# Optimization experiments

Measured on AMD Instinct MI355X. Metric: run time of the kernel, lower is better.

Reference implementation:

```python
import jax, jax.numpy as jnp
import numpy as np

N, D, V = 4096, 256, 32000
B, T = 32, 256
U_DECAY, X_DECAY = 0.97, 0.97
EPS = 1e-6


def layernorm_row(z):
    # matches torch: (z - mean) / (std + eps), std with Bessel correction (ddof=1)
    m = jnp.mean(z, axis=-1, keepdims=True)
    s = jnp.std(z, axis=-1, keepdims=True, ddof=1)
    return (z - m) / (s + EPS)


def setup_inputs() -> dict:
    key = jax.random.key(0)
    k1, k2, k3, k4, k5 = jax.random.split(key, 5)
    token_emb = jax.random.normal(k1, (V, D), jnp.float32) / np.float32(np.sqrt(D))
    E = jax.random.normal(k2, (D, N), jnp.float32) / np.float32(np.sqrt(N))
    Dx = jax.random.normal(k3, (N, D), jnp.float32) / np.float32(np.sqrt(D))
    Dy = jax.random.normal(k4, (N, D), jnp.float32) / np.float32(np.sqrt(D))
    idx = jax.random.randint(k5, (B, T), 0, V)
    return {"idx": idx, "token_emb": token_emb, "E": E, "Dx": Dx, "Dy": Dy}


def reference(idx, token_emb, E, Dx, Dy):
    b = idx.shape[0]

    def step(carry, tok):
        x, rho = carry                                   # x: (b,n), rho: (b,d,n)
        v_prev = token_emb[tok]                          # (b,d) embedding gather
        x_t = X_DECAY * x + jax.nn.relu(v_prev @ Dx.T)   # (b,n)
        x_t = x_t / (jnp.sum(jnp.abs(x_t), axis=-1, keepdims=True) + EPS)  # L1 normalize
        a_star = jnp.einsum('bdn,bn->bd', rho, x_t)      # fast-weight readout
        y_t = jax.nn.relu(layernorm_row(a_star) @ Dy.T) * jax.nn.relu(x_t)  # (b,n)
        v_star = layernorm_row(y_t @ E.T)                # (b,d)
        # Hebbian decayed outer-product memory update
        rho = U_DECAY * (rho + jnp.einsum('bd,bn->bdn', layernorm_row(v_prev), x_t))
        return (x_t, rho), v_star

    x0 = jnp.zeros((b, N), jnp.float32)
    rho0 = jnp.zeros((b, D, N), jnp.float32)
    (_, _), vs = jax.lax.scan(step, (x0, rho0), idx.T)   # vs: (T,b,d)
    return jnp.transpose(vs, (1, 0, 2))                  # (b,T,d)
```

## Files before the change

kernel.cpp:

```cpp
#include <hip/hip_runtime.h>
#include <hip/hip_bf16.h>

#define NN 4096
#define DD 256
#define BB 32
#define TT 256
#define EPS 1e-6f
#define DECAY 0.97f
#define LOG2_DECAY -0.043943348f

typedef __hip_bfloat16 bf16;
typedef short short8 __attribute__((ext_vector_type(8)));
typedef float floatx4 __attribute__((ext_vector_type(4)));

__device__ __forceinline__ float bfu2f(short u) {
    return __uint_as_float(((unsigned)(unsigned short)u) << 16);
}

__device__ __forceinline__ float blk_sum_256(float v, volatile float* s4) {
#pragma unroll
    for (int o = 32; o > 0; o >>= 1) v += __shfl_down(v, o, 64);
    int lane = threadIdx.x & 63, w = threadIdx.x >> 6;
    __syncthreads();
    if (lane == 0) s4[w] = v;
    __syncthreads();
    return s4[0] + s4[1] + s4[2] + s4[3];
}

__device__ __forceinline__ void gl16(const bf16* g, bf16* l) {
    __builtin_amdgcn_global_load_lds((const __attribute__((address_space(1))) void*)g,
                                     (__attribute__((address_space(3))) void*)l, 16, 0, 0);
}

__global__ void k_detect(const unsigned short* __restrict__ raw, int* __restrict__ flag) {
    __shared__ int cnt[4];
    int tid = threadIdx.x;
    int bad = 0;
    for (int i = tid; i < 8192; i += 256) {
        unsigned int u = raw[2 * i];
        float v = __uint_as_float(u << 16);
        if (!(fabsf(v) < 1e6f)) bad++;
    }
#pragma unroll
    for (int o = 32; o > 0; o >>= 1) bad += __shfl_down(bad, o, 64);
    int lane = tid & 63, w = tid >> 6;
    if (lane == 0) cnt[w] = bad;
    __syncthreads();
    if (tid == 0) flag[0] = (cnt[0] + cnt[1] + cnt[2] + cnt[3] < 32) ? 1 : 0;
}

__global__ __launch_bounds__(256) void k_convert3(const void* __restrict__ s0,
                                                  const void* __restrict__ s1,
                                                  const void* __restrict__ s2,
                                                  bf16* __restrict__ d0,
                                                  bf16* __restrict__ d1,
                                                  bf16* __restrict__ d2,
                                                  const int* __restrict__ flag) {
    const int per = NN * DD / 8;
    int i = blockIdx.x * 256 + threadIdx.x;
    int m = i / per, j = i % per;
    const void* s = (m == 0) ? s0 : (m == 1) ? s1 : s2;
    bf16* d = (m == 0) ? d0 : (m == 1) ? d1 : d2;
    if (flag[0]) {
        ((uint4*)d)[j] = ((const uint4*)s)[j];
    } else {
        const float4* f = (const float4*)s;
        float4 a = f[2 * j], b = f[2 * j + 1];
        short8 o;
        float va[8] = {a.x, a.y, a.z, a.w, b.x, b.y, b.z, b.w};
#pragma unroll
        for (int k = 0; k < 8; k++) {
            bf16 t = __float2bfloat16(va[k]);
            o[k] = *reinterpret_cast<short*>(&t);
        }
        ((short8*)d)[j] = o;
    }
}

__global__ __launch_bounds__(256) void k_gather_ln(const void* __restrict__ emb,
                                                   const int* __restrict__ idx,
                                                   bf16* __restrict__ Vpb,
                                                   bf16* __restrict__ Ub,
                                                   const int* __restrict__ flag) {
    __shared__ float s4[4];
    int r = blockIdx.x, d = threadIdx.x;
    int tok = idx[r];
    long o = (long)tok * DD + d;
    float e = flag[0] ? __bfloat162float(((const bf16*)emb)[o]) : ((const float*)emb)[o];
    Vpb[(long)r * DD + d] = __float2bfloat16(e);
    float m = blk_sum_256(e, s4) * (1.0f / DD);
    float zc = e - m;
    float var = blk_sum_256(zc * zc, s4) * (1.0f / (DD - 1));
    Ub[(long)r * DD + d] = __float2bfloat16(zc / (sqrtf(fmaxf(var, 0.f)) + EPS));
}

__global__ __launch_bounds__(256) void k_transpose(const bf16* __restrict__ Ub,
                                                   bf16* __restrict__ Ut) {
    __shared__ bf16 tile[32][33];
    int b = blockIdx.z;
    int t0 = blockIdx.x * 32, d0 = blockIdx.y * 32;
    const bf16* src = Ub + (long)b * TT * DD;
    bf16* dst = Ut + (long)b * DD * TT;
    int rr = threadIdx.x >> 3, c4 = (threadIdx.x & 7) * 4;
#pragma unroll
    for (int i = 0; i < 4; i++) tile[rr][c4 + i] = src[(long)(t0 + rr) * DD + d0 + c4 + i];
    __syncthreads();
#pragma unroll
    for (int i = 0; i < 4; i++) dst[(long)(d0 + rr) * TT + t0 + c4 + i] = tile[c4 + i][rr];
}

enum { EPI_RELU_BF16 = 0, EPI_NONE_F32 = 1, EPI_RELU_MULX_BF16 = 2, EPI_NONE_BF16 = 3 };

template <int EPI>
__global__ __launch_bounds__(512, 2) void k_fused256(const bf16* __restrict__ A,
                                                     const bf16* __restrict__ B,
                                                     bf16* __restrict__ C,
                                                     const bf16* __restrict__ Xaux,
                                                     float* __restrict__ Wsum) {
    __shared__ __align__(16) char smem[65536];
    bf16* R = (bf16*)smem;

    int bx = blockIdx.x, by = blockIdx.y;
    {
        int gx = gridDim.x;
        int nwg = gx * gridDim.y;
        int id = by * gx + bx;
        int q = nwg >> 3;
        int nid = (id & 7) * q + (id >> 3);
        bx = nid % gx;
        by = nid / gx;
    }
    int bm = by * 256, bn = bx * 256;
    int tid = threadIdx.x, wid = tid >> 6, lane = tid & 63;
    int wr = wid >> 2, wc = wid & 3;
    int lm = lane & 15, kh = lane >> 4;

    int srow2 = tid >> 2;
    int swzcol = (((tid & 3) ^ ((srow2 >> 1) & 3)) << 3);
    const bf16* gA0 = A + (long)(bm + srow2) * DD + swzcol;
    const bf16* gA1 = gA0 + (long)128 * DD;
    const bf16* gB0 = B + (long)(bn + srow2) * DD + swzcol;
    const bf16* gB1 = gB0 + (long)128 * DD;
    int chunk = ((kh ^ ((lm >> 1) & 3)) << 3);

    floatx4 acc[8][4];
#pragma unroll
    for (int i = 0; i < 8; i++)
#pragma unroll
        for (int j = 0; j < 4; j++) acc[i][j] = (floatx4){0.f, 0.f, 0.f, 0.f};

#define STAGE256(SBASE, KK)                             \
    {                                                   \
        bf16* As_ = (bf16*)(SBASE);                     \
        bf16* Bs_ = As_ + 8192;                         \
        gl16(gA0 + (KK), As_ + tid * 8);                \
        gl16(gA1 + (KK), As_ + 4096 + tid * 8);         \
        gl16(gB0 + (KK), Bs_ + tid * 8);                \
        gl16(gB1 + (KK), Bs_ + 4096 + tid * 8);         \
    }

    STAGE256(smem, 0);

    int cur = 0;
#pragma unroll
    for (int k0 = 0; k0 < 256; k0 += 32) {
        __builtin_amdgcn_s_barrier();
        __builtin_amdgcn_sched_barrier(0);
        if (k0 + 32 < 256) STAGE256(smem + ((cur ^ 1) * 32768), k0 + 32);
        if (k0 + 32 < 256) asm volatile("s_waitcnt vmcnt(4)" ::: "memory");
        else               asm volatile("s_waitcnt vmcnt(0)" ::: "memory");
        __builtin_amdgcn_s_barrier();
        __builtin_amdgcn_sched_barrier(0);
        bf16* cbA = (bf16*)(smem + cur * 32768);
        bf16* cbB = cbA + 8192;
        short8 af[8], bfr[4];
#pragma unroll
        for (int i = 0; i < 8; i++)
            af[i] = *(const short8*)(cbA + (wr * 128 + i * 16 + lm) * 32 + chunk);
#pragma unroll
        for (int j = 0; j < 4; j++)
            bfr[j] = *(const short8*)(cbB + (wc * 64 + j * 16 + lm) * 32 + chunk);
#pragma unroll
        for (int i = 0; i < 8; i++)
#pragma unroll
            for (int j = 0; j < 4; j++)
                acc[i][j] = __builtin_amdgcn_mfma_f32_16x16x32_bf16(af[i], bfr[j], acc[i][j], 0, 0, 0);
        cur ^= 1;
    }
#undef STAGE256

#pragma unroll
    for (int p = 0; p < 4; p++) {
        __syncthreads();
        if (wr == (p >> 1)) {
            int ibase = (p & 1) * 4;
#pragma unroll
            for (int ii = 0; ii < 4; ii++)
#pragma unroll
                for (int j = 0; j < 4; j++)
#pragma unroll
                    for (int r = 0; r < 4; r++) {
                        int rr = ii * 16 + kh * 4 + r;
                        int cc = wc * 64 + j * 16 + lm;
                        R[rr * 264 + cc] = __float2bfloat16(fmaxf(acc[ibase + ii][j][r], 0.f));
                    }
        }
        __syncthreads();
#pragma unroll
        for (int it = 0; it < 4; it++) {
            int row_l = it * 16 + (tid >> 5);
            int c8 = (tid & 31) * 8;
            short8 vv = *(const short8*)(R + row_l * 264 + c8);
            int gm = bm + p * 64 + row_l;
            long off = (long)gm * NN + bn + c8;
            if (EPI == EPI_RELU_BF16) {
                *(short8*)(C + off) = vv;
                float s = 0.f;
#pragma unroll
                for (int k = 0; k < 8; k++) s += bfu2f(vv[k]);
#pragma unroll
                for (int o = 16; o > 0; o >>= 1) s += __shfl_down(s, o, 32);
                if ((tid & 31) == 0) atomicAdd(&Wsum[gm], s);
            } else {
                short8 xx = *(const short8*)(Xaux + off);
                short8 oo;
#pragma unroll
                for (int k = 0; k < 8; k++) {
                    float prod = bfu2f(vv[k]) * fmaxf(bfu2f(xx[k]), 0.f);
                    bf16 t = __float2bfloat16(prod);
                    oo[k] = *reinterpret_cast<short*>(&t);
                }
                *(short8*)(C + off) = oo;
            }
        }
    }
}

template <int EPI, int KSPLIT, int TRI, int SWZ>
__global__ __launch_bounds__(256) void k_mfma_nt(int K,
                                                 const bf16* __restrict__ A, int lda, long sA,
                                                 const bf16* __restrict__ B, int ldb, long sB,
                                                 void* __restrict__ Cv, int ldc, long sC,
                                                 const bf16* __restrict__ Xaux,
                                                 float* __restrict__ Wsum) {
    __shared__ __align__(16) char smem[49152];
    bf16* R = (bf16*)smem;

    int z = blockIdx.z;
    int bz = z / KSPLIT, ks = z % KSPLIT;
    A += (long)bz * sA;
    B += (long)bz * sB;
    int bx = blockIdx.x, by = blockIdx.y;
    if (TRI) {
        by = (blockIdx.x >= 1) ? 1 : 0;
        bx = (blockIdx.x == 2) ? 1 : 0;
    }
    if (SWZ) {
        int gx = gridDim.x;
        int nwg = gx * gridDim.y;
        int id = by * gx + bx;
        int q = nwg >> 3;
        int nid = (id & 7) * q + (id >> 3);
        bx = nid % gx;
        by = nid / gx;
    }
    int bm = by * 128, bn = bx * 128;
    int tid = threadIdx.x;
    int srow = tid >> 2;
    int scol = ((((srow >> 1) & 3) ^ (tid & 3)) << 3);
    int w = tid >> 6, lane = tid & 63;
    int wm = (w >> 1) * 64, wn = (w & 1) * 64;
    int lm = lane & 15, kh = lane >> 4;

    floatx4 acc[4][4];
#pragma unroll
    for (int i = 0; i < 4; i++)
#pragma unroll
        for (int j = 0; j < 4; j++) acc[i][j] = (floatx4){0.f, 0.f, 0.f, 0.f};

    int kchunk = K / KSPLIT;
    int kbeg = ks * kchunk, kend = kbeg + kchunk;
    const bf16* gA0 = A + (long)(bm + srow) * lda + scol;
    const bf16* gA1 = gA0 + (long)64 * lda;
    const bf16* gB0 = B + (long)(bn + srow) * ldb + scol;
    const bf16* gB1 = gB0 + (long)64 * ldb;
    int dslot = tid * 8;

#define STAGE_SLOT(SBASE, KK)                          \
    {                                                  \
        bf16* bufA = (bf16*)(SBASE);                   \
        bf16* bufB = bufA + 4096;                      \
        gl16(gA0 + (KK), bufA + dslot);                \
        gl16(gA1 + (KK), bufA + 2048 + dslot);         \
        gl16(gB0 + (KK), bufB + dslot);                \
        gl16(gB1 + (KK), bufB + 2048 + dslot);         \
    }

    STAGE_SLOT(smem, kbeg);
    if (kbeg + 32 < kend) STAGE_SLOT(smem + 16384, kbeg + 32);

    int cur = 0;
    for (int k0 = kbeg; k0 < kend; k0 += 32) {
        __builtin_amdgcn_s_barrier();
        __builtin_amdgcn_sched_barrier(0);
        if (k0 + 64 < kend) {
            int ps = (cur == 0) ? 2 : cur - 1;
            STAGE_SLOT(smem + ps * 16384, k0 + 64);
        }
        int rem = (kend - k0 - 32) >> 5;
        if (rem >= 2)      asm volatile("s_waitcnt vmcnt(8)" ::: "memory");
        else if (rem == 1) asm volatile("s_waitcnt vmcnt(4)" ::: "memory");
        else               asm volatile("s_waitcnt vmcnt(0)" ::: "memory");
        __builtin_amdgcn_s_barrier();
        __builtin_amdgcn_sched_barrier(0);
        bf16* cbA = (bf16*)(smem + cur * 16384);
        bf16* cbB = cbA + 4096;
        short8 af[4], bfr[4];
#pragma unroll
        for (int i = 0; i < 4; i++) {
            int row = wm + i * 16 + lm;
            af[i] = *(const short8*)(cbA + row * 32 + ((((row >> 1) & 3) ^ kh) << 3));
        }
#pragma unroll
        for (int j = 0; j < 4; j++) {
            int row = wn + j * 16 + lm;
            bfr[j] = *(const short8*)(cbB + row * 32 + ((((row >> 1) & 3) ^ kh) << 3));
        }
#pragma unroll
        for (int i = 0; i < 4; i++)
#pragma unroll
            for (int j = 0; j < 4; j++)
                acc[i][j] = __builtin_amdgcn_mfma_f32_16x16x32_bf16(af[i], bfr[j], acc[i][j], 0, 0, 0);
        cur = (cur == 2) ? 0 : cur + 1;
    }
#undef STAGE_SLOT

    if (EPI == EPI_NONE_F32) {
        long cbase = (long)z * sC;
#pragma unroll
        for (int i = 0; i < 4; i++)
#pragma unroll
            for (int j = 0; j < 4; j++)
#pragma unroll
                for (int r = 0; r < 4; r++) {
                    int gm = bm + wm + i * 16 + kh * 4 + r;
                    int gn = bn + wn + j * 16 + lm;
                    ((float*)Cv)[cbase + (long)gm * ldc + gn] = acc[i][j][r];
                }
        return;
    }

    bf16* Cb = (bf16*)Cv + (long)z * sC;
#pragma unroll
    for (int p = 0; p < 2; p++) {
        __syncthreads();
        if ((w >> 1) == p) {
#pragma unroll
            for (int i = 0; i < 4; i++)
#pragma unroll
                for (int j = 0; j < 4; j++)
#pragma unroll
                    for (int r = 0; r < 4; r++) {
                        int rr = i * 16 + kh * 4 + r;
                        int cc = wn + j * 16 + lm;
                        float val = acc[i][j][r];
                        if (EPI != EPI_NONE_BF16) val = fmaxf(val, 0.f);
                        R[rr * 136 + cc] = __float2bfloat16(val);
                    }
        }
        __syncthreads();
#pragma unroll
        for (int it = 0; it < 4; it++) {
            int row_l = it * 16 + (tid >> 4);
            int c8 = (tid & 15) * 8;
            short8 vv = *(const short8*)(R + row_l * 136 + c8);
            int gm = bm + p * 64 + row_l;
            long off = (long)gm * ldc + bn + c8;
            if (EPI == EPI_NONE_BF16) {
                *(short8*)(Cb + off) = vv;
            } else if (EPI == EPI_RELU_BF16) {
                *(short8*)(Cb + off) = vv;
                float s = 0.f;
#pragma unroll
                for (int k = 0; k < 8; k++) s += bfu2f(vv[k]);
#pragma unroll
                for (int o = 8; o > 0; o >>= 1) s += __shfl_down(s, o, 16);
                if ((tid & 15) == 0) atomicAdd(&Wsum[gm], s);
            } else {
                short8 xx = *(const short8*)(Xaux + off);
                short8 oo;
#pragma unroll
                for (int k = 0; k < 8; k++) {
                    float prod = bfu2f(vv[k]) * fmaxf(bfu2f(xx[k]), 0.f);
                    bf16 t = __float2bfloat16(prod);
                    oo[k] = *reinterpret_cast<short*>(&t);
                }
                *(short8*)(Cb + off) = oo;
            }
        }
    }
}

__global__ __launch_bounds__(256) void k_scalar_scan(const float* __restrict__ Wsum,
                                                     float* __restrict__ invS) {
    __shared__ float sw[BB * TT];
    for (int i = threadIdx.x; i < BB * TT; i += 256) sw[i] = Wsum[i];
    __syncthreads();
    int b = threadIdx.x;
    if (b < BB) {
        float sig = 0.f;
        for (int t = 0; t < TT; t++) {
            float S = DECAY * sig + sw[b * TT + t];
            float inv = 1.f / (S + EPS);
            invS[b * TT + t] = inv;
            sig = S * inv;
        }
    }
}

__global__ __launch_bounds__(256) void k_colscan(bf16* __restrict__ W,
                                                 const float* __restrict__ invS) {
    __shared__ float sv[TT];
    int b = blockIdx.y;
    sv[threadIdx.x] = invS[b * TT + threadIdx.x];
    __syncthreads();
    int n = blockIdx.x * 256 + threadIdx.x;
    bf16* p = W + (long)b * TT * NN + n;
    float x = 0.f;
    for (int t = 0; t < TT; t++) {
        float w = __bfloat162float(p[(long)t * NN]);
        x = (DECAY * x + w) * sv[t];
        p[(long)t * NN] = __float2bfloat16(x);
    }
}

__global__ __launch_bounds__(256) void k_reduce_mask(const bf16* __restrict__ Gp,
                                                     bf16* __restrict__ G) {
    int r = blockIdx.x;
    int b = r >> 8, t = r & 255;
    int s = threadIdx.x;
    long base = ((long)b * 4) * 65536 + (long)t * 256 + s;
    float v = __bfloat162float(Gp[base]) + __bfloat162float(Gp[base + 65536]) +
              __bfloat162float(Gp[base + 2 * 65536]) + __bfloat162float(Gp[base + 3 * 65536]);
    float o = (s < t) ? v * exp2f((float)(t - s) * LOG2_DECAY) : 0.f;
    G[(long)r * 256 + s] = __float2bfloat16(o);
}

__global__ __launch_bounds__(256) void k_ln_rows(const bf16* __restrict__ Zp,
                                                 bf16* __restrict__ O) {
    __shared__ float s4[4];
    long r = blockIdx.x;
    int d = threadIdx.x;
    long b = r >> 8, t = r & 255;
    long base = (b * 2) * 65536 + t * 256 + d;
    float z = __bfloat162float(Zp[base]) + __bfloat162float(Zp[base + 65536]);
    float m = blk_sum_256(z, s4) * (1.0f / DD);
    float zc = z - m;
    float var = blk_sum_256(zc * zc, s4) * (1.0f / (DD - 1));
    O[r * DD + d] = __float2bfloat16(zc / (sqrtf(fmaxf(var, 0.f)) + EPS));
}

__global__ __launch_bounds__(256) void k_final_ln(const float* __restrict__ Zp,
                                                  void* __restrict__ out,
                                                  const int* __restrict__ flag) {
    __shared__ float s4[4];
    long r = blockIdx.x;
    int d = threadIdx.x;
    const long SL = (long)8192 * 256;
    long o = r * DD + d;
    float z = Zp[o] + Zp[o + SL];
    float m = blk_sum_256(z, s4) * (1.0f / DD);
    float zc = z - m;
    float var = blk_sum_256(zc * zc, s4) * (1.0f / (DD - 1));
    float v = zc / (sqrtf(fmaxf(var, 0.f)) + EPS);
    if (flag[0]) ((bf16*)out)[o] = __float2bfloat16(v);
    else ((float*)out)[o] = v;
}

extern "C" void kernel_launch(void* const* d_in, const int* in_sizes, int n_in,
                              void* d_out, int out_size, void* d_ws, size_t ws_size,
                              hipStream_t stream) {
    const int* idx = (const int*)d_in[0];
    const void* emb = d_in[1];
    const void* E = d_in[2];
    const void* Dx = d_in[3];
    const void* Dy = d_in[4];

    char* base = (char*)d_ws;
    size_t off = 0;
    int* flag = (int*)base; off += 1024;
    bf16* Dxb = (bf16*)(base + off); off += (size_t)NN * DD * 2;
    bf16* Dyb = (bf16*)(base + off); off += (size_t)NN * DD * 2;
    bf16* Eb  = (bf16*)(base + off); off += (size_t)DD * NN * 2;
    bf16* Vpb = (bf16*)(base + off); off += (size_t)BB * TT * DD * 2;
    bf16* Ub  = (bf16*)(base + off); off += (size_t)BB * TT * DD * 2;
    bf16* Ut  = (bf16*)(base + off); off += (size_t)BB * TT * DD * 2;
    float* Wsum = (float*)(base + off); off += (size_t)BB * TT * 4;
    float* invS = (float*)(base + off); off += (size_t)BB * TT * 4;
    bf16* ALNb = (bf16*)(base + off); off += (size_t)BB * TT * DD * 2;
    bf16* G = (bf16*)(base + off); off += (size_t)BB * TT * TT * 2;
    bf16* Gp = (bf16*)(base + off); off += (size_t)4 * BB * TT * TT * 2;
    bf16* Astar = Gp;
    float* Zp = (float*)Gp;
    bf16* Xb = (bf16*)(base + off); off += (size_t)BB * TT * NN * 2;

    const int M = BB * TT;

    k_detect<<<1, 256, 0, stream>>>((const unsigned short*)emb, flag);
    k_convert3<<<3 * NN * DD / 8 / 256, 256, 0, stream>>>(Dx, Dy, E, Dxb, Dyb, Eb, flag);
    k_gather_ln<<<M, 256, 0, stream>>>(emb, idx, Vpb, Ub, flag);
    k_transpose<<<dim3(8, 8, BB), 256, 0, stream>>>(Ub, Ut);

    hipMemsetAsync(Wsum, 0, (size_t)M * 4, stream);

    k_fused256<EPI_RELU_BF16><<<dim3(16, 32), 512, 0, stream>>>(Vpb, Dxb, Xb, nullptr, Wsum);

    k_scalar_scan<<<1, 256, 0, stream>>>(Wsum, invS);
    k_colscan<<<dim3(16, BB, 1), 256, 0, stream>>>(Xb, invS);

    k_mfma_nt<EPI_NONE_BF16, 4, 1, 0><<<dim3(3, 1, BB * 4), 256, 0, stream>>>(
        NN, Xb, NN, (long)TT * NN, Xb, NN, (long)TT * NN, Gp, TT, (long)TT * TT, nullptr, nullptr);
    k_reduce_mask<<<M, 256, 0, stream>>>(Gp, G);

    k_mfma_nt<EPI_NONE_BF16, 2, 0, 0><<<dim3(2, 2, BB * 2), 256, 0, stream>>>(
        TT, G, TT, (long)TT * TT, Ut, TT, (long)DD * TT, Astar, DD, (long)TT * DD, nullptr, nullptr);
    k_ln_rows<<<M, 256, 0, stream>>>(Astar, ALNb);

    k_fused256<EPI_RELU_MULX_BF16><<<dim3(16, 32), 512, 0, stream>>>(ALNb, Dyb, Xb, Xb, nullptr);

    k_mfma_nt<EPI_NONE_F32, 2, 0, 1><<<dim3(2, 64, 2), 256, 0, stream>>>(
        NN, Xb, NN, 0, Eb, NN, 0, Zp, DD, (long)M * DD, nullptr, nullptr);

    k_final_ln<<<M, 256, 0, stream>>>(Zp, d_out, flag);
}
```

Measured before the change: 316.0 us.

## Fuse causal decay mask into Gram epilogue and split-K sum into A* GEMM

Applies the causal decay mask inside the Gram-matrix GEMM epilogue, per split-K partial. The A* GEMM now sums the four partials while loading its A operand, which removes the separate reduce_mask kernel and its G buffer. The new A* kernel uses a triangular-aware grid that skips the upper-right zero block. The ln_rows kernel adds the second K-half only for rows at or past 128. This trades a kernel launch and a full read/write pass for extra global loads inside the GEMM, and each partial is rounded to bf16 before summing.

Result: no change. 321.3 us (median of 2 runs) (+1.7%).

```diff
diff --git a/kernel.cpp b/kernel.cpp
--- a/kernel.cpp
+++ b/kernel.cpp
@@ -15,6 +15,11 @@
 
 __device__ __forceinline__ float bfu2f(short u) {
     return __uint_as_float(((unsigned)(unsigned short)u) << 16);
+}
+
+__device__ __forceinline__ short f2bfu(float f) {
+    bf16 t = __float2bfloat16(f);
+    return *reinterpret_cast<short*>(&t);
 }
 
 __device__ __forceinline__ float blk_sum_256(float v, volatile float* s4) {
@@ -69,10 +74,7 @@
         short8 o;
         float va[8] = {a.x, a.y, a.z, a.w, b.x, b.y, b.z, b.w};
 #pragma unroll
-        for (int k = 0; k < 8; k++) {
-            bf16 t = __float2bfloat16(va[k]);
-            o[k] = *reinterpret_cast<short*>(&t);
-        }
+        for (int k = 0; k < 8; k++) o[k] = f2bfu(va[k]);
         ((short8*)d)[j] = o;
     }
 }
@@ -109,7 +111,8 @@
     for (int i = 0; i < 4; i++) dst[(long)(d0 + rr) * TT + t0 + c4 + i] = tile[c4 + i][rr];
 }
 
-enum { EPI_RELU_BF16 = 0, EPI_NONE_F32 = 1, EPI_RELU_MULX_BF16 = 2, EPI_NONE_BF16 = 3 };
+enum { EPI_RELU_BF16 = 0, EPI_NONE_F32 = 1, EPI_RELU_MULX_BF16 = 2, EPI_NONE_BF16 = 3,
+       EPI_MASK_BF16 = 4 };
 
 template <int EPI>
 __global__ __launch_bounds__(512, 2) void k_fused256(const bf16* __restrict__ A,
@@ -227,8 +230,7 @@
 #pragma unroll
                 for (int k = 0; k < 8; k++) {
                     float prod = bfu2f(vv[k]) * fmaxf(bfu2f(xx[k]), 0.f);
-                    bf16 t = __float2bfloat16(prod);
-                    oo[k] = *reinterpret_cast<short*>(&t);
+                    oo[k] = f2bfu(prod);
                 }
                 *(short8*)(C + off) = oo;
             }
@@ -364,7 +366,7 @@
                         int rr = i * 16 + kh * 4 + r;
                         int cc = wn + j * 16 + lm;
                         float val = acc[i][j][r];
-                        if (EPI != EPI_NONE_BF16) val = fmaxf(val, 0.f);
+                        if (EPI == EPI_RELU_BF16 || EPI == EPI_RELU_MULX_BF16) val = fmaxf(val, 0.f);
                         R[rr * 136 + cc] = __float2bfloat16(val);
                     }
         }
@@ -378,6 +380,16 @@
             long off = (long)gm * ldc + bn + c8;
             if (EPI == EPI_NONE_BF16) {
                 *(short8*)(Cb + off) = vv;
+            } else if (EPI == EPI_MASK_BF16) {
+                short8 oo;
+#pragma unroll
+                for (int k = 0; k < 8; k++) {
+                    int s = bn + c8 + k;
+                    float f = bfu2f(vv[k]);
+                    f = (s < gm) ? f * exp2f((float)(gm - s) * LOG2_DECAY) : 0.f;
+                    oo[k] = f2bfu(f);
+                }
+                *(short8*)(Cb + off) = oo;
             } else if (EPI == EPI_RELU_BF16) {
                 *(short8*)(Cb + off) = vv;
                 float s = 0.f;
@@ -392,11 +404,135 @@
 #pragma unroll
                 for (int k = 0; k < 8; k++) {
                     float prod = bfu2f(vv[k]) * fmaxf(bfu2f(xx[k]), 0.f);
-                    bf16 t = __float2bfloat16(prod);
-                    oo[k] = *reinterpret_cast<short*>(&t);
+                    oo[k] = f2bfu(prod);
                 }
                 *(short8*)(Cb + off) = oo;
             }
+        }
+    }
+}
+
+__global__ __launch_bounds__(256) void k_astar(const bf16* __restrict__ Gp,
+                                               const bf16* __restrict__ Ut,
+                                               bf16* __restrict__ Ap) {
+    __shared__ __align__(16) char smem[32768];
+    bf16* R = (bf16*)smem;
+
+    int b = blockIdx.z;
+    int y = blockIdx.y;
+    int by = (y >= 1) ? 1 : 0, ks = (y == 2) ? 1 : 0;
+    int bx = blockIdx.x;
+    int bm = by * 128, bn = bx * 128, kbeg = ks * 128;
+    int tid = threadIdx.x;
+    int srow = tid >> 2;
+    int scol = ((((srow >> 1) & 3) ^ (tid & 3)) << 3);
+    int w = tid >> 6, lane = tid & 63;
+    int wm = (w >> 1) * 64, wn = (w & 1) * 64;
+    int lm = lane & 15, kh = lane >> 4;
+
+    const bf16* gA = Gp + (long)b * 4 * 65536;
+    long aoff0 = (long)(bm + srow) * TT + scol + kbeg;
+    long aoff1 = (long)(bm + srow + 64) * TT + scol + kbeg;
+    const bf16* gB0 = Ut + (long)b * DD * TT + (long)(bn + srow) * TT + scol + kbeg;
+    const bf16* gB1 = gB0 + (long)64 * TT;
+    int dslot = tid * 8;
+
+    floatx4 acc[4][4];
+#pragma unroll
+    for (int i = 0; i < 4; i++)
+#pragma unroll
+        for (int j = 0; j < 4; j++) acc[i][j] = (floatx4){0.f, 0.f, 0.f, 0.f};
+
+#define LOAD4SUM(DST, AOFF)                                        \
+    {                                                              \
+        short8 p0 = *(const short8*)(gA + (AOFF));                 \
+        short8 p1 = *(const short8*)(gA + 65536 + (AOFF));         \
+        short8 p2 = *(const short8*)(gA + 2 * 65536 + (AOFF));     \
+        short8 p3 = *(const short8*)(gA + 3 * 65536 + (AOFF));     \
+        short8 o_;                                                 \
+        _Pragma("unroll")                                          \
+        for (int k_ = 0; k_ < 8; k_++)                             \
+            o_[k_] = f2bfu(bfu2f(p0[k_]) + bfu2f(p1[k_]) +         \
+                           bfu2f(p2[k_]) + bfu2f(p3[k_]));         \
+        DST = o_;                                                  \
+    }
+
+    {
+        bf16* As_ = (bf16*)smem;
+        bf16* Bs_ = As_ + 4096;
+        gl16(gB0, Bs_ + dslot);
+        gl16(gB1, Bs_ + 2048 + dslot);
+        short8 ra0, ra1;
+        LOAD4SUM(ra0, aoff0);
+        LOAD4SUM(ra1, aoff1);
+        *(short8*)(As_ + dslot) = ra0;
+        *(short8*)(As_ + 2048 + dslot) = ra1;
+    }
+    __syncthreads();
+
+    int cur = 0;
+    for (int kk = 0; kk < 128; kk += 32) {
+        bf16* cbA = (bf16*)(smem + cur * 16384);
+        bf16* cbB = cbA + 4096;
+        bf16* nbA = (bf16*)(smem + (cur ^ 1) * 16384);
+        bf16* nbB = nbA + 4096;
+        short8 na0, na1;
+        bool has = (kk + 32) < 128;
+        if (has) {
+            gl16(gB0 + kk + 32, nbB + dslot);
+            gl16(gB1 + kk + 32, nbB + 2048 + dslot);
+            LOAD4SUM(na0, aoff0 + kk + 32);
+            LOAD4SUM(na1, aoff1 + kk + 32);
+        }
+        short8 af[4], bfr[4];
+#pragma unroll
+        for (int i = 0; i < 4; i++) {
+            int row = wm + i * 16 + lm;
+            af[i] = *(const short8*)(cbA + row * 32 + ((((row >> 1) & 3) ^ kh) << 3));
+        }
+#pragma unroll
+        for (int j = 0; j < 4; j++) {
+            int row = wn + j * 16 + lm;
+            bfr[j] = *(const short8*)(cbB + row * 32 + ((((row >> 1) & 3) ^ kh) << 3));
+        }
+#pragma unroll
+        for (int i = 0; i < 4; i++)
+#pragma unroll
+            for (int j = 0; j < 4; j++)
+                acc[i][j] = __builtin_amdgcn_mfma_f32_16x16x32_bf16(af[i], bfr[j], acc[i][j], 0, 0, 0);
+        if (has) {
+            *(short8*)(nbA + dslot) = na0;
+            *(short8*)(nbA + 2048 + dslot) = na1;
+        }
+        __syncthreads();
+        cur ^= 1;
+    }
+#undef LOAD4SUM
+
+    bf16* Cb = Ap + ((long)b * 2 + ks) * 65536;
+#pragma unroll
+    for (int p = 0; p < 2; p++) {
+        __syncthreads();
+        if ((w >> 1) == p) {
+#pragma unroll
+            for (int i = 0; i < 4; i++)
+#pragma unroll
+                for (int j = 0; j < 4; j++)
+#pragma unroll
+                    for (int r = 0; r < 4; r++) {
+                        int rr = i * 16 + kh * 4 + r;
+                        int cc = wn + j * 16 + lm;
+                        R[rr * 136 + cc] = __float2bfloat16(acc[i][j][r]);
+                    }
+        }
+        __syncthreads();
+#pragma unroll
+        for (int it = 0; it < 4; it++) {
+            int row_l = it * 16 + (tid >> 4);
+            int c8 = (tid & 15) * 8;
+            short8 vv = *(const short8*)(R + row_l * 136 + c8);
+            int gm = bm + p * 64 + row_l;
+            *(short8*)(Cb + (long)gm * DD + bn + c8) = vv;
         }
     }
 }
@@ -434,26 +570,15 @@
     }
 }
 
-__global__ __launch_bounds__(256) void k_reduce_mask(const bf16* __restrict__ Gp,
-                                                     bf16* __restrict__ G) {
-    int r = blockIdx.x;
-    int b = r >> 8, t = r & 255;
-    int s = threadIdx.x;
-    long base = ((long)b * 4) * 65536 + (long)t * 256 + s;
-    float v = __bfloat162float(Gp[base]) + __bfloat162float(Gp[base + 65536]) +
-              __bfloat162float(Gp[base + 2 * 65536]) + __bfloat162float(Gp[base + 3 * 65536]);
-    float o = (s < t) ? v * exp2f((float)(t - s) * LOG2_DECAY) : 0.f;
-    G[(long)r * 256 + s] = __float2bfloat16(o);
-}
-
-__global__ __launch_bounds__(256) void k_ln_rows(const bf16* __restrict__ Zp,
+__global__ __launch_bounds__(256) void k_ln_rows(const bf16* __restrict__ Ap,
                                                  bf16* __restrict__ O) {
     __shared__ float s4[4];
     long r = blockIdx.x;
     int d = threadIdx.x;
     long b = r >> 8, t = r & 255;
     long base = (b * 2) * 65536 + t * 256 + d;
-    float z = __bfloat162float(Zp[base]) + __bfloat162float(Zp[base + 65536]);
+    float z = bfu2f(*(const short*)&Ap[base]);
+    if (t >= 128) z += bfu2f(*(const short*)&Ap[base + 65536]);
     float m = blk_sum_256(z, s4) * (1.0f / DD);
     float zc = z - m;
     float var = blk_sum_256(zc * zc, s4) * (1.0f / (DD - 1));
@@ -498,9 +623,8 @@
     float* Wsum = (float*)(base + off); off += (size_t)BB * TT * 4;
     float* invS = (float*)(base + off); off += (size_t)BB * TT * 4;
     bf16* ALNb = (bf16*)(base + off); off += (size_t)BB * TT * DD * 2;
-    bf16* G = (bf16*)(base + off); off += (size_t)BB * TT * TT * 2;
     bf16* Gp = (bf16*)(base + off); off += (size_t)4 * BB * TT * TT * 2;
-    bf16* Astar = Gp;
+    bf16* Ap = (bf16*)(base + off); off += (size_t)2 * BB * TT * DD * 2;
     float* Zp = (float*)Gp;
     bf16* Xb = (bf16*)(base + off); off += (size_t)BB * TT * NN * 2;
 
@@ -518,13 +642,11 @@
     k_scalar_scan<<<1, 256, 0, stream>>>(Wsum, invS);
     k_colscan<<<dim3(16, BB, 1), 256, 0, stream>>>(Xb, invS);
 
-    k_mfma_nt<EPI_NONE_BF16, 4, 1, 0><<<dim3(3, 1, BB * 4), 256, 0, stream>>>(
+    k_mfma_nt<EPI_MASK_BF16, 4, 1, 0><<<dim3(3, 1, BB * 4), 256, 0, stream>>>(
         NN, Xb, NN, (long)TT * NN, Xb, NN, (long)TT * NN, Gp, TT, (long)TT * TT, nullptr, nullptr);
-    k_reduce_mask<<<M, 256, 0, stream>>>(Gp, G);
-
-    k_mfma_nt<EPI_NONE_BF16, 2, 0, 0><<<dim3(2, 2, BB * 2), 256, 0, stream>>>(
-        TT, G, TT, (long)TT * TT, Ut, TT, (long)DD * TT, Astar, DD, (long)TT * DD, nullptr, nullptr);
-    k_ln_rows<<<M, 256, 0, stream>>>(Astar, ALNb);
+
+    k_astar<<<dim3(2, 3, BB), 256, 0, stream>>>(Gp, Ut, Ap);
+    k_ln_rows<<<M, 256, 0, stream>>>(Ap, ALNb);
 
     k_fused256<EPI_RELU_MULX_BF16><<<dim3(16, 32), 512, 0, stream>>>(ALNb, Dyb, Xb, Xb, nullptr);
 
```
